# Optimization experiments

Measured on AMD Instinct MI355X. Metric: run time of the kernel, lower is better.

The kernel has to match this reference:

```python
import jax, jax.numpy as jnp
import numpy as np

B, S, H, W, E, NH = 8, 16, 32, 32, 128, 8
HD = E // NH
EPS = 1e-5


def setup_inputs() -> dict:
    key = jax.random.key(0)
    ks = jax.random.split(key, 6)
    sc = lambda fan: 1.0 / np.sqrt(fan).astype(np.float32)
    return {
        "inputs": jax.random.normal(ks[0], (B, S, H, W, E), jnp.float32),
        "W_proj": jax.random.normal(ks[1], (E, E), jnp.float32) * sc(E),
        "ln_gamma": jnp.ones((E,), jnp.float32),
        "ln_beta": jnp.zeros((E,), jnp.float32),
        "W_in": jax.random.normal(ks[2], (E, 3 * E), jnp.float32) * sc(E),
        "W_out": jax.random.normal(ks[3], (E, E), jnp.float32) * sc(E),
        "conv_k": jax.random.normal(ks[4], (4 * E, 2 * E, 3, 3), jnp.float32) * sc(2 * E * 9),
    }


def reference(inputs, W_proj, ln_gamma, ln_beta, W_in, W_out, conv_k):
    # x = silu(project(inputs))
    x = jax.nn.silu(inputs @ W_proj)
    # LayerNorm over last dim
    mu = x.mean(-1, keepdims=True)
    var = x.var(-1, keepdims=True)
    x = (x - mu) * jax.lax.rsqrt(var + EPS) * ln_gamma + ln_beta
    # Multi-head attention over the sequence dim, batched over (b, h, w)
    qkv = (x @ W_in).reshape(B, S, H, W, NH, 3 * HD)
    q, k, v = jnp.split(qkv, 3, axis=-1)
    scale = 1.0 / np.sqrt(HD).astype(np.float32)
    scores = jnp.einsum('bshwid,blhwid->bhwisl', q, k) * scale  # (B,H,W,NH,S,S)
    tril = jnp.tril(jnp.ones((S, S), jnp.float32))
    # faithful to source: +1.0 on/below diagonal, -1000.0 above
    mask = tril * 1.0 + (1.0 - tril) * (-1000.0)
    attnw = jax.nn.softmax(scores + mask, axis=-1)
    ao = jnp.einsum('bhwisl,blhwid->bshwid', attnw, v).reshape(B, S, H, W, E)
    x = ao @ W_out + inputs  # residual
    # ConvLSTM over seq: (B,S,H,W,E) -> (S,B,E,H,W) for scan
    xc = jnp.transpose(x, (1, 0, 4, 2, 3))
    h0 = jnp.zeros((B, E, H, W), x.dtype)
    c0 = jnp.zeros((B, E, H, W), x.dtype)

    def step(carry, xt):
        h, c = carry
        comb = jnp.concatenate([xt, h], axis=1)  # (B, 2E, H, W)
        cc = jax.lax.conv_general_dilated(
            comb, conv_k, window_strides=(1, 1), padding='SAME',
            dimension_numbers=('NCHW', 'OIHW', 'NCHW'))
        ci, cf, co, cg = jnp.split(cc, 4, axis=1)
        c_next = jax.nn.sigmoid(cf) * c + jax.nn.sigmoid(ci) * jnp.tanh(cg)
        h_next = jax.nn.sigmoid(co) * jnp.tanh(c_next)
        return (h_next, c_next), h_next

    _, outs = jax.lax.scan(step, (h0, c0), xc)  # (S,B,E,H,W)
    return jnp.transpose(outs, (1, 0, 3, 4, 2))  # (B,S,H,W,E)
```

## Files before the change

kernel.cpp:

```cpp
#include <hip/hip_runtime.h>
#include <math.h>

#define B_  8
#define S_  16
#define H_  32
#define W_  32
#define E_  128
#define NH_ 8
#define HD_ 16
#define HW_ (H_*W_)
#define NTOK (B_*S_*H_*W_)

typedef __attribute__((ext_vector_type(8))) short short8;
typedef __attribute__((ext_vector_type(4))) short short4v;
typedef __attribute__((ext_vector_type(4))) float floatx4;

__device__ __forceinline__ float sigf(float x){
    return 1.f/(1.f+__expf(-x));
}
__device__ __forceinline__ float tanh_fast(float x){
    x = fminf(fmaxf(x, -15.f), 15.f);
    float e = __expf(2.f*x);
    return (e-1.f)/(e+1.f);
}
__device__ __forceinline__ unsigned short f2bf(float f){
    unsigned int u = __float_as_uint(f);
    u = (u + 0x7fffu + ((u >> 16) & 1u)) >> 16;
    return (unsigned short)u;
}
__device__ __forceinline__ float bf2f(unsigned short h){
    return __uint_as_float(((unsigned int)h) << 16);
}

__device__ __forceinline__ void st_gate(float* p, float v){ *p = v; }
__device__ __forceinline__ void st_gate(unsigned short* p, float v){ *p = f2bf(v); }
__device__ __forceinline__ void load_gate(const float* p, float* o){
    float4 v = *(const float4*)p; o[0]=v.x; o[1]=v.y; o[2]=v.z; o[3]=v.w;
}
__device__ __forceinline__ void load_gate(const unsigned short* p, float* o){
    ushort4 v = *(const ushort4*)p;
    o[0]=bf2f(v.x); o[1]=bf2f(v.y); o[2]=bf2f(v.z); o[3]=bf2f(v.w);
}

__global__ __launch_bounds__(256)
void k_pack_wproj(const float* __restrict__ Wp, short* __restrict__ Wpp){
    int p = blockIdx.x*256 + threadIdx.x;
    int L = p & 63;
    int idx = p >> 6;
    int nt = idx / 12, kb = idx - nt*12;
    int n = nt*16 + (L & 15);
    int kr = (kb & 3)*32 + (L >> 4)*8;
    bool lo = (kb >= 8);
    short8 v;
    #pragma unroll
    for (int j=0;j<8;j++){
        float wv = Wp[(kr+j)*128 + n];
        unsigned short h = f2bf(wv);
        v[j] = lo ? (short)f2bf(wv - bf2f(h)) : (short)h;
    }
    *(short8*)&Wpp[(long)p*8] = v;
}

__global__ __launch_bounds__(256,4)
void k_proj_ln_mfma(const float* __restrict__ in, const short* __restrict__ Wpp,
                    const float* __restrict__ gamma, const float* __restrict__ beta,
                    float* __restrict__ X){
    __shared__ short As[64*264];
    __shared__ float red[4][64][2];
    int tid = threadIdx.x;
    int w = tid >> 6, L = tid & 63;
    int quad = L >> 4, lm = L & 15;
    long r0 = (long)blockIdx.x * 64;

    {
        int c = (tid & 31)*4;
        int rbase = tid >> 5;
        #pragma unroll
        for (int rr=0; rr<8; rr++){
            int r = rr*8 + rbase;
            float4 v = *(const float4*)&in[(r0 + r)*128 + c];
            short4v hv, lv;
            unsigned short h;
            h = f2bf(v.x); hv[0]=(short)h; lv[0]=(short)f2bf(v.x - bf2f(h));
            h = f2bf(v.y); hv[1]=(short)h; lv[1]=(short)f2bf(v.y - bf2f(h));
            h = f2bf(v.z); hv[2]=(short)h; lv[2]=(short)f2bf(v.z - bf2f(h));
            h = f2bf(v.w); hv[3]=(short)h; lv[3]=(short)f2bf(v.w - bf2f(h));
            *(short4v*)&As[r*264 + c] = hv;
            *(short4v*)&As[r*264 + 128 + c] = lv;
        }
    }
    __syncthreads();

    floatx4 acc[4][2];
    #pragma unroll
    for (int mtl=0;mtl<4;mtl++)
        #pragma unroll
        for (int nti=0;nti<2;nti++)
            acc[mtl][nti] = (floatx4){0.f,0.f,0.f,0.f};
    const short8* Bp8 = (const short8*)Wpp;
    #pragma unroll
    for (int kb=0; kb<12; kb++){
        int off = (kb<4) ? kb*32 : ((kb<8) ? 128+(kb-4)*32 : (kb-8)*32);
        short8 af[4];
        #pragma unroll
        for (int mtl=0;mtl<4;mtl++)
            af[mtl] = *(const short8*)&As[(mtl*16+lm)*264 + off + quad*8];
        #pragma unroll
        for (int nti=0;nti<2;nti++){
            short8 bf = Bp8[((2*w+nti)*12+kb)*64 + L];
            #pragma unroll
            for (int mtl=0;mtl<4;mtl++)
                acc[mtl][nti] = __builtin_amdgcn_mfma_f32_16x16x32_bf16(af[mtl], bf, acc[mtl][nti], 0,0,0);
        }
    }

    #pragma unroll
    for (int mtl=0;mtl<4;mtl++){
        float p1[4]={0,0,0,0}, p2[4]={0,0,0,0};
        #pragma unroll
        for (int nti=0;nti<2;nti++)
            #pragma unroll
            for (int r=0;r<4;r++){
                float a = acc[mtl][nti][r];
                float si = a*sigf(a);
                acc[mtl][nti][r] = si;
                p1[r] += si; p2[r] += si*si;
            }
        #pragma unroll
        for (int d=1; d<16; d<<=1)
            #pragma unroll
            for (int r=0;r<4;r++){
                p1[r] += __shfl_xor(p1[r], d);
                p2[r] += __shfl_xor(p2[r], d);
            }
        if (lm == 0){
            #pragma unroll
            for (int r=0;r<4;r++){
                int row = mtl*16 + quad*4 + r;
                red[w][row][0] = p1[r];
                red[w][row][1] = p2[r];
            }
        }
    }
    __syncthreads();
    float g[2], bb[2];
    #pragma unroll
    for (int nti=0;nti<2;nti++){
        g[nti]  = gamma[(2*w+nti)*16 + lm];
        bb[nti] = beta [(2*w+nti)*16 + lm];
    }
    #pragma unroll
    for (int mtl=0;mtl<4;mtl++){
        #pragma unroll
        for (int r=0;r<4;r++){
            int row = mtl*16 + quad*4 + r;
            float s1 = red[0][row][0] + red[1][row][0] + red[2][row][0] + red[3][row][0];
            float s2 = red[0][row][1] + red[1][row][1] + red[2][row][1] + red[3][row][1];
            float mu  = s1 * (1.f/128.f);
            float var = s2 * (1.f/128.f) - mu*mu;
            float rs  = rsqrtf(var + 1e-5f);
            #pragma unroll
            for (int nti=0;nti<2;nti++)
                X[(r0+row)*128 + (2*w+nti)*16 + lm] = (acc[mtl][nti][r]-mu)*rs*g[nti] + bb[nti];
        }
    }
}

__global__ __launch_bounds__(256)
void k_pack_win(const float* __restrict__ Win, short* __restrict__ Winp){
    int p = blockIdx.x*256 + threadIdx.x;
    int L = p & 63;
    int idx = p >> 6;
    int nt = idx >> 2, kc = idx & 3;
    int n = nt*16 + (L & 15);
    int k0 = kc*32 + (L >> 4)*8;
    short8 v;
    #pragma unroll
    for (int j=0;j<8;j++) v[j] = (short)f2bf(Win[(k0+j)*384 + n]);
    *(short8*)&Winp[(long)p*8] = v;
}

__global__ __launch_bounds__(256)
void k_pack_wout(const float* __restrict__ Wout, short* __restrict__ Woutp){
    int p = blockIdx.x*256 + threadIdx.x;
    int L = p & 63;
    int idx = p >> 6;
    int h = idx >> 3, nt = idx & 7;
    int n = nt*16 + (L & 15);
    int k0 = (L >> 4)*8;
    short8 v;
    #pragma unroll
    for (int j=0;j<8;j++){
        int k = k0 + j;
        v[j] = (k < 16) ? (short)f2bf(Wout[(h*16+k)*128 + n]) : (short)0;
    }
    *(short8*)&Woutp[(long)p*8] = v;
}

__global__ __launch_bounds__(256,5)
void k_attn_mfma(const float* __restrict__ X, const short* __restrict__ Winp,
                 const short* __restrict__ Woutp, const float* __restrict__ resid,
                 float* __restrict__ Y){
    __shared__ short lds[16000];
    const int XO=0;
    const int QO=8704;
    const int KO=10240;
    const int VO=11776;
    const int PO=12928;
    const int AOO=14464;
    int tid = threadIdx.x;
    int w = tid >> 6, L = tid & 63;
    int quad = L >> 4, lm = L & 15;
    int b = blockIdx.x >> 8, tile = blockIdx.x & 255;
    int hw0 = tile * 4;
    int hw = hw0 + w;

    {
        int cq = L & 31, rh = L >> 5;
        for (int p=0; p<8; p++){
            int m = w*16 + p*2 + rh;
            int s = m & 15;
            float4 v = *(const float4*)&X[((((long)b*16 + s)*1024) + hw)*128 + cq*4];
            short4v hv;
            hv[0]=(short)f2bf(v.x); hv[1]=(short)f2bf(v.y);
            hv[2]=(short)f2bf(v.z); hv[3]=(short)f2bf(v.w);
            *(short4v*)&lds[XO + m*136 + cq*4] = hv;
        }
    }

    floatx4 Oa[8];
    #pragma unroll
    for (int nt=0;nt<8;nt++) Oa[nt] = (floatx4){0.f,0.f,0.f,0.f};

    const floatx4 zc = (floatx4){0.f,0.f,0.f,0.f};
    const short8 z8 = {0,0,0,0,0,0,0,0};
    int m0 = w*16;

    for (int h=0; h<8; h++){
        floatx4 qacc[3];
        #pragma unroll
        for (int t=0;t<3;t++) qacc[t] = zc;
        #pragma unroll
        for (int kc=0;kc<4;kc++){
            short8 af = *(const short8*)&lds[XO + (m0+lm)*136 + kc*32 + quad*8];
            #pragma unroll
            for (int t=0;t<3;t++){
                int nt = 3*h + t;
                short8 bf = *(const short8*)&Winp[(long)((nt*4+kc)*64 + L)*8];
                qacc[t] = __builtin_amdgcn_mfma_f32_16x16x32_bf16(af, bf, qacc[t], 0,0,0);
            }
        }
        #pragma unroll
        for (int r=0;r<4;r++){
            lds[QO + (m0+quad*4+r)*24 + lm] = (short)f2bf(qacc[0][r]);
            lds[KO + (m0+quad*4+r)*24 + lm] = (short)f2bf(qacc[1][r]);
        }
        {
            short4v vv;
            #pragma unroll
            for (int r=0;r<4;r++) vv[r] = (short)f2bf(qacc[2][r]);
            *(short4v*)&lds[VO + lm*72 + m0 + quad*4] = vv;
        }

        {
            short8 qf = z8, kf = z8;
            if (quad < 2){
                qf = *(const short8*)&lds[QO + (m0+lm)*24 + quad*8];
                kf = *(const short8*)&lds[KO + (m0+lm)*24 + quad*8];
            }
            floatx4 scv = __builtin_amdgcn_mfma_f32_16x16x32_bf16(qf, kf, zc, 0,0,0);
            float pv[4], mr[4];
            #pragma unroll
            for (int r=0;r<4;r++){
                int si = quad*4 + r;
                pv[r] = scv[r]*0.25f + (lm <= si ? 1.0f : -1000.0f);
                mr[r] = pv[r];
            }
            #pragma unroll
            for (int d=1; d<16; d<<=1)
                #pragma unroll
                for (int r=0;r<4;r++) mr[r] = fmaxf(mr[r], __shfl_xor(mr[r], d));
            float ex[4], sm[4];
            #pragma unroll
            for (int r=0;r<4;r++){ ex[r] = __expf(pv[r]-mr[r]); sm[r] = ex[r]; }
            #pragma unroll
            for (int d=1; d<16; d<<=1)
                #pragma unroll
                for (int r=0;r<4;r++) sm[r] += __shfl_xor(sm[r], d);
            #pragma unroll
            for (int r=0;r<4;r++)
                lds[PO + (m0+quad*4+r)*24 + lm] = (short)f2bf(ex[r]/sm[r]);

            short8 pf = z8, vf = z8;
            if (quad < 2){
                pf = *(const short8*)&lds[PO + (m0+lm)*24 + quad*8];
                vf = *(const short8*)&lds[VO + lm*72 + m0 + quad*8];
            }
            floatx4 aov = __builtin_amdgcn_mfma_f32_16x16x32_bf16(pf, vf, zc, 0,0,0);
            #pragma unroll
            for (int r=0;r<4;r++)
                lds[AOO + (m0+quad*4+r)*24 + lm] = (short)f2bf(aov[r]);
        }

        {
            short8 aof = z8;
            if (quad < 2)
                aof = *(const short8*)&lds[AOO + (m0+lm)*24 + quad*8];
            #pragma unroll
            for (int nt=0;nt<8;nt++){
                short8 wf = *(const short8*)&Woutp[(long)((h*8+nt)*64 + L)*8];
                Oa[nt] = __builtin_amdgcn_mfma_f32_16x16x32_bf16(aof, wf, Oa[nt], 0,0,0);
            }
        }
    }

    #pragma unroll
    for (int nt=0;nt<8;nt++){
        int n = nt*16 + lm;
        #pragma unroll
        for (int r=0;r<4;r++){
            int s = quad*4 + r;
            long addr = (((long)b*16 + s)*1024 + hw)*128 + n;
            Y[addr] = Oa[nt][r] + resid[addr];
        }
    }
}

__global__ __launch_bounds__(256)
void k_pack_w(const float* __restrict__ ck, short* __restrict__ Bp){
    int p = blockIdx.x*256 + threadIdx.x;
    int L = p & 63;
    int nt = (p >> 6) & 31;
    int c32 = (p >> 11) & 7;
    int tap = p >> 14;
    int oc = nt*16 + (L & 15);
    int kq = L >> 4;
    short8 v;
    #pragma unroll
    for (int j=0;j<8;j++){
        int ic = c32*32 + kq*8 + j;
        v[j] = (short)f2bf(ck[(oc*256+ic)*9 + tap]);
    }
    *(short8*)&Bp[(long)p*8] = v;
}

__global__ __launch_bounds__(256)
void k_pack_x(const float* __restrict__ X, short* __restrict__ xh, int s, int zero_h){
    int idx = blockIdx.x*256 + threadIdx.x;
    int row = idx >> 4;
    int ch = (idx & 15) * 8;
    int b = row >> 10, hw = row & 1023;
    const float* src = X + (((long)(b*16+s)*1024 + hw)*128 + ch);
    float4 a = *(const float4*)src;
    float4 c = *(const float4*)(src+4);
    short8 v;
    v[0]=(short)f2bf(a.x); v[1]=(short)f2bf(a.y); v[2]=(short)f2bf(a.z); v[3]=(short)f2bf(a.w);
    v[4]=(short)f2bf(c.x); v[5]=(short)f2bf(c.y); v[6]=(short)f2bf(c.z); v[7]=(short)f2bf(c.w);
    *(short8*)&xh[(long)row*256 + ch] = v;
    if (zero_h){
        short8 z = {0,0,0,0,0,0,0,0};
        *(short8*)&xh[(long)row*256 + 128 + ch] = z;
    }
}

template<typename GT>
__global__ __launch_bounds__(512,2)
void k_conv_mfma(const short* __restrict__ xh, const short* __restrict__ Bp,
                 GT* __restrict__ gbuf){
    __shared__ short As[6*34*264];
    int tid = threadIdx.x;
    int Nblk = blockIdx.x & 3, g = blockIdx.x >> 2;
    int b = g >> 3, y0 = (g & 7)*4;
    int w = tid >> 6, L = tid & 63;
    int quad = L >> 4, lm = L & 15;
    int wm = w >> 1, wn = w & 1;
    int ntg = Nblk*8 + wn*4;

    const short8 z8 = {0,0,0,0,0,0,0,0};
    {
        short8 vs[13];
        #pragma unroll
        for (int i=0; i<13; i++){
            int pidx = i*512 + tid;
            short8 v = z8;
            if (pidx < 6528){
                int cb  = pidx & 31;
                int pos = pidx >> 5;
                int row = pos / 34;
                int xp  = pos - row*34;
                int yy = y0 - 1 + row, xx = xp - 1;
                if (yy>=0 && yy<32 && xx>=0 && xx<32)
                    v = *(const short8*)&xh[(((long)(b*32+yy)*32+xx)<<8) + cb*8];
            }
            vs[i] = v;
        }
        #pragma unroll
        for (int i=0; i<13; i++){
            int pidx = i*512 + tid;
            if (pidx < 6528){
                int cb  = pidx & 31;
                int pos = pidx >> 5;
                *(short8*)&As[pos*264 + cb*8] = vs[i];
            }
        }
    }
    __syncthreads();

    floatx4 acc[2][4];
    #pragma unroll
    for (int mtl=0;mtl<2;mtl++)
        #pragma unroll
        for (int nti=0;nti<4;nti++)
            acc[mtl][nti] = (floatx4){0.f,0.f,0.f,0.f};

    const short8* Bp8 = (const short8*)Bp;

    for (int tap=0; tap<9; tap++){
        int dy = tap/3 - 1, dx = tap - (tap/3)*3 - 1;
        int abase[2];
        #pragma unroll
        for (int mtl=0;mtl<2;mtl++){
            int x = mtl*16 + lm;
            abase[mtl] = (((wm+dy+1)*34) + x + dx + 1)*264 + quad*8;
        }
        #pragma unroll
        for (int sic=0; sic<4; sic++){
            #pragma unroll
            for (int c2=0; c2<2; c2++){
                short8 bfr[4];
                #pragma unroll
                for (int nti=0;nti<4;nti++)
                    bfr[nti] = Bp8[((tap*8 + sic*2 + c2)*32 + ntg + nti)*64 + L];
                #pragma unroll
                for (int mtl=0;mtl<2;mtl++){
                    short8 afr = *(const short8*)&As[abase[mtl] + sic*64 + c2*32];
                    #pragma unroll
                    for (int nti=0;nti<4;nti++)
                        acc[mtl][nti] = __builtin_amdgcn_mfma_f32_16x16x32_bf16(afr, bfr[nti], acc[mtl][nti], 0,0,0);
                }
            }
        }
    }

    #pragma unroll
    for (int mtl=0;mtl<2;mtl++){
        #pragma unroll
        for (int nti=0;nti<4;nti++){
            int n = Nblk*128 + (wn*4+nti)*16 + lm;
            #pragma unroll
            for (int r=0;r<4;r++){
                long row = (long)g*128 + wm*32 + mtl*16 + quad*4 + r;
                st_gate(&gbuf[row*512 + n], acc[mtl][nti][r]);
            }
        }
    }
}

template<typename GT>
__global__ __launch_bounds__(256)
void k_lstm(const GT* __restrict__ gbuf, float* __restrict__ cbuf,
            float* __restrict__ X, short* __restrict__ xh, int s){
    int idx = blockIdx.x*256 + threadIdx.x;
    int row = idx >> 5;
    int c4 = (idx & 31)*4;
    float gi[4], gf[4], go[4], gg[4];
    const GT* gp = gbuf + (long)row*512 + c4;
    load_gate(gp,       gi);
    load_gate(gp + 128, gf);
    load_gate(gp + 256, go);
    load_gate(gp + 384, gg);
    float co[4];
    if (s == 0){ co[0]=co[1]=co[2]=co[3]=0.f; }
    else {
        float4 cv = *(const float4*)&cbuf[(long)row*128 + c4];
        co[0]=cv.x; co[1]=cv.y; co[2]=cv.z; co[3]=cv.w;
    }
    float cn[4], hn[4];
    #pragma unroll
    for (int j=0;j<4;j++){
        cn[j] = sigf(gf[j])*co[j] + sigf(gi[j])*tanh_fast(gg[j]);
        hn[j] = sigf(go[j])*tanh_fast(cn[j]);
    }
    *(float4*)&cbuf[(long)row*128 + c4] = make_float4(cn[0],cn[1],cn[2],cn[3]);
    int b = row >> 10, hw = row & 1023;
    long xoff = (((long)(b*16+s)*1024 + hw)*128) + c4;
    *(float4*)&X[xoff] = make_float4(hn[0],hn[1],hn[2],hn[3]);
    ushort4 hv;
    hv.x = f2bf(hn[0]); hv.y = f2bf(hn[1]); hv.z = f2bf(hn[2]); hv.w = f2bf(hn[3]);
    *(ushort4*)&xh[(long)row*256 + 128 + c4] = hv;
    if (s < 15){
        long x2 = (((long)(b*16+s+1)*1024 + hw)*128) + c4;
        float4 xv = *(const float4*)&X[x2];
        ushort4 xb;
        xb.x = f2bf(xv.x); xb.y = f2bf(xv.y); xb.z = f2bf(xv.z); xb.w = f2bf(xv.w);
        *(ushort4*)&xh[(long)row*256 + c4] = xb;
    }
}

extern "C" void kernel_launch(void* const* d_in, const int* in_sizes, int n_in,
                              void* d_out, int out_size, void* d_ws, size_t ws_size,
                              hipStream_t stream){
    const float* inputs = (const float*)d_in[0];
    const float* Wp     = (const float*)d_in[1];
    const float* gamma  = (const float*)d_in[2];
    const float* beta   = (const float*)d_in[3];
    const float* Win    = (const float*)d_in[4];
    const float* Wout   = (const float*)d_in[5];
    const float* ck     = (const float*)d_in[6];
    float* X = (float*)d_out;

    char* ws = (char*)d_ws;
    const size_t szB    = 147456ull*16;
    const size_t szXH   = 8192ull*256*2;
    const size_t szC    = 8192ull*128*4;
    const size_t szWin  = 6144ull*16;
    const size_t szWout = 4096ull*16;
    short* Bp    = (short*)(ws);
    short* xh    = (short*)(ws + szB);
    float* cbuf  = (float*)(ws + szB + szXH);
    short* Winp  = (short*)(ws + szB + szXH + szC);
    short* Woutp = (short*)(ws + szB + szXH + szC + szWin);
    char*  gch   =         ws + szB + szXH + szC + szWin + szWout;
    bool gate_f32 = ws_size >= (szB + szXH + szC + szWin + szWout + 8192ull*512*4);
    short* Wprojp = (short*)gch;

    k_pack_w<<<576, 256, 0, stream>>>(ck, Bp);
    k_pack_win<<<24, 256, 0, stream>>>(Win, Winp);
    k_pack_wout<<<16, 256, 0, stream>>>(Wout, Woutp);
    k_pack_wproj<<<24, 256, 0, stream>>>(Wp, Wprojp);
    k_proj_ln_mfma<<<NTOK/64, 256, 0, stream>>>(inputs, Wprojp, gamma, beta, X);
    k_attn_mfma<<<2048, 256, 0, stream>>>(X, Winp, Woutp, inputs, X);
    k_pack_x<<<512, 256, 0, stream>>>(X, xh, 0, 1);

    if (gate_f32){
        float* gbuf = (float*)gch;
        for (int s=0; s<16; s++){
            k_conv_mfma<float><<<256, 512, 0, stream>>>(xh, Bp, gbuf);
            k_lstm<float><<<1024, 256, 0, stream>>>(gbuf, cbuf, X, xh, s);
        }
    } else {
        unsigned short* gbuf = (unsigned short*)gch;
        for (int s=0; s<16; s++){
            k_conv_mfma<unsigned short><<<256, 512, 0, stream>>>(xh, Bp, gbuf);
            k_lstm<unsigned short><<<1024, 256, 0, stream>>>(gbuf, cbuf, X, xh, s);
        }
    }
}
```

Measured before the change: 859.7 us.

## Fuse ConvLSTM gate convolution with LSTM cell update using ping-pong state buffers

```diff
diff --git a/kernel.cpp b/kernel.cpp
--- a/kernel.cpp
+++ b/kernel.cpp
@@ -30,16 +30,6 @@
 }
 __device__ __forceinline__ float bf2f(unsigned short h){
     return __uint_as_float(((unsigned int)h) << 16);
-}
-
-__device__ __forceinline__ void st_gate(float* p, float v){ *p = v; }
-__device__ __forceinline__ void st_gate(unsigned short* p, float v){ *p = f2bf(v); }
-__device__ __forceinline__ void load_gate(const float* p, float* o){
-    float4 v = *(const float4*)p; o[0]=v.x; o[1]=v.y; o[2]=v.z; o[3]=v.w;
-}
-__device__ __forceinline__ void load_gate(const unsigned short* p, float* o){
-    ushort4 v = *(const ushort4*)p;
-    o[0]=bf2f(v.x); o[1]=bf2f(v.y); o[2]=bf2f(v.z); o[3]=bf2f(v.w);
 }
 
 __global__ __launch_bounds__(256)
@@ -363,10 +353,10 @@
     }
 }
 
-template<typename GT>
 __global__ __launch_bounds__(512,2)
-void k_conv_mfma(const short* __restrict__ xh, const short* __restrict__ Bp,
-                 GT* __restrict__ gbuf){
+void k_conv_lstm(const short* __restrict__ xh_in, const short* __restrict__ Bp,
+                 float* __restrict__ cbuf, float* __restrict__ X,
+                 short* __restrict__ xh_out, int s){
     __shared__ short As[6*34*264];
     int tid = threadIdx.x;
     int Nblk = blockIdx.x & 3, g = blockIdx.x >> 2;
@@ -374,7 +364,6 @@
     int w = tid >> 6, L = tid & 63;
     int quad = L >> 4, lm = L & 15;
     int wm = w >> 1, wn = w & 1;
-    int ntg = Nblk*8 + wn*4;
 
     const short8 z8 = {0,0,0,0,0,0,0,0};
     {
@@ -390,7 +379,7 @@
                 int xp  = pos - row*34;
                 int yy = y0 - 1 + row, xx = xp - 1;
                 if (yy>=0 && yy<32 && xx>=0 && xx<32)
-                    v = *(const short8*)&xh[(((long)(b*32+yy)*32+xx)<<8) + cb*8];
+                    v = *(const short8*)&xh_in[(((long)(b*32+yy)*32+xx)<<8) + cb*8];
             }
             vs[i] = v;
         }
@@ -410,8 +399,8 @@
     #pragma unroll
     for (int mtl=0;mtl<2;mtl++)
         #pragma unroll
-        for (int nti=0;nti<4;nti++)
-            acc[mtl][nti] = (floatx4){0.f,0.f,0.f,0.f};
+        for (int q=0;q<4;q++)
+            acc[mtl][q] = (floatx4){0.f,0.f,0.f,0.f};
 
     const short8* Bp8 = (const short8*)Bp;
 
@@ -429,71 +418,40 @@
             for (int c2=0; c2<2; c2++){
                 short8 bfr[4];
                 #pragma unroll
-                for (int nti=0;nti<4;nti++)
-                    bfr[nti] = Bp8[((tap*8 + sic*2 + c2)*32 + ntg + nti)*64 + L];
+                for (int q=0;q<4;q++)
+                    bfr[q] = Bp8[((tap*8 + sic*2 + c2)*32 + q*8 + Nblk*2 + wn)*64 + L];
                 #pragma unroll
                 for (int mtl=0;mtl<2;mtl++){
                     short8 afr = *(const short8*)&As[abase[mtl] + sic*64 + c2*32];
                     #pragma unroll
-                    for (int nti=0;nti<4;nti++)
-                        acc[mtl][nti] = __builtin_amdgcn_mfma_f32_16x16x32_bf16(afr, bfr[nti], acc[mtl][nti], 0,0,0);
+                    for (int q=0;q<4;q++)
+                        acc[mtl][q] = __builtin_amdgcn_mfma_f32_16x16x32_bf16(afr, bfr[q], acc[mtl][q], 0,0,0);
                 }
             }
         }
     }
 
+    int ch = Nblk*32 + wn*16 + lm;
     #pragma unroll
     for (int mtl=0;mtl<2;mtl++){
         #pragma unroll
-        for (int nti=0;nti<4;nti++){
-            int n = Nblk*128 + (wn*4+nti)*16 + lm;
-            #pragma unroll
-            for (int r=0;r<4;r++){
-                long row = (long)g*128 + wm*32 + mtl*16 + quad*4 + r;
-                st_gate(&gbuf[row*512 + n], acc[mtl][nti][r]);
-            }
-        }
-    }
-}
-
-template<typename GT>
-__global__ __launch_bounds__(256)
-void k_lstm(const GT* __restrict__ gbuf, float* __restrict__ cbuf,
-            float* __restrict__ X, short* __restrict__ xh, int s){
-    int idx = blockIdx.x*256 + threadIdx.x;
-    int row = idx >> 5;
-    int c4 = (idx & 31)*4;
-    float gi[4], gf[4], go[4], gg[4];
-    const GT* gp = gbuf + (long)row*512 + c4;
-    load_gate(gp,       gi);
-    load_gate(gp + 128, gf);
-    load_gate(gp + 256, go);
-    load_gate(gp + 384, gg);
-    float co[4];
-    if (s == 0){ co[0]=co[1]=co[2]=co[3]=0.f; }
-    else {
-        float4 cv = *(const float4*)&cbuf[(long)row*128 + c4];
-        co[0]=cv.x; co[1]=cv.y; co[2]=cv.z; co[3]=cv.w;
-    }
-    float cn[4], hn[4];
-    #pragma unroll
-    for (int j=0;j<4;j++){
-        cn[j] = sigf(gf[j])*co[j] + sigf(gi[j])*tanh_fast(gg[j]);
-        hn[j] = sigf(go[j])*tanh_fast(cn[j]);
-    }
-    *(float4*)&cbuf[(long)row*128 + c4] = make_float4(cn[0],cn[1],cn[2],cn[3]);
-    int b = row >> 10, hw = row & 1023;
-    long xoff = (((long)(b*16+s)*1024 + hw)*128) + c4;
-    *(float4*)&X[xoff] = make_float4(hn[0],hn[1],hn[2],hn[3]);
-    ushort4 hv;
-    hv.x = f2bf(hn[0]); hv.y = f2bf(hn[1]); hv.z = f2bf(hn[2]); hv.w = f2bf(hn[3]);
-    *(ushort4*)&xh[(long)row*256 + 128 + c4] = hv;
-    if (s < 15){
-        long x2 = (((long)(b*16+s+1)*1024 + hw)*128) + c4;
-        float4 xv = *(const float4*)&X[x2];
-        ushort4 xb;
-        xb.x = f2bf(xv.x); xb.y = f2bf(xv.y); xb.z = f2bf(xv.z); xb.w = f2bf(xv.w);
-        *(ushort4*)&xh[(long)row*256 + c4] = xb;
+        for (int r=0;r<4;r++){
+            long row = (long)g*128 + wm*32 + mtl*16 + quad*4 + r;
+            float co = (s == 0) ? 0.f : cbuf[row*128 + ch];
+            float gi = acc[mtl][0][r], gf = acc[mtl][1][r];
+            float go = acc[mtl][2][r], gg = acc[mtl][3][r];
+            float cn = sigf(gf)*co + sigf(gi)*tanh_fast(gg);
+            float hn = sigf(go)*tanh_fast(cn);
+            cbuf[row*128 + ch] = cn;
+            int b2 = (int)(row >> 10), hw = (int)(row & 1023);
+            long xoff = (((long)(b2*16+s)*1024 + hw)*128) + ch;
+            X[xoff] = hn;
+            xh_out[row*256 + 128 + ch] = (short)f2bf(hn);
+            if (s < 15){
+                long x2 = (((long)(b2*16+s+1)*1024 + hw)*128) + ch;
+                xh_out[row*256 + ch] = (short)f2bf(X[x2]);
+            }
+        }
     }
 }
 
@@ -516,13 +474,12 @@
     const size_t szWin  = 6144ull*16;
     const size_t szWout = 4096ull*16;
     short* Bp    = (short*)(ws);
-    short* xh    = (short*)(ws + szB);
+    short* xh0   = (short*)(ws + szB);
     float* cbuf  = (float*)(ws + szB + szXH);
     short* Winp  = (short*)(ws + szB + szXH + szC);
     short* Woutp = (short*)(ws + szB + szXH + szC + szWin);
-    char*  gch   =         ws + szB + szXH + szC + szWin + szWout;
-    bool gate_f32 = ws_size >= (szB + szXH + szC + szWin + szWout + 8192ull*512*4);
-    short* Wprojp = (short*)gch;
+    short* xh1   = (short*)(ws + szB + szXH + szC + szWin + szWout);
+    short* Wprojp= (short*)(ws + szB + szXH + szC + szWin + szWout + szXH);
 
     k_pack_w<<<576, 256, 0, stream>>>(ck, Bp);
     k_pack_win<<<24, 256, 0, stream>>>(Win, Winp);
@@ -530,19 +487,11 @@
     k_pack_wproj<<<24, 256, 0, stream>>>(Wp, Wprojp);
     k_proj_ln_mfma<<<NTOK/64, 256, 0, stream>>>(inputs, Wprojp, gamma, beta, X);
     k_attn_mfma<<<2048, 256, 0, stream>>>(X, Winp, Woutp, inputs, X);
-    k_pack_x<<<512, 256, 0, stream>>>(X, xh, 0, 1);
-
-    if (gate_f32){
-        float* gbuf = (float*)gch;
-        for (int s=0; s<16; s++){
-            k_conv_mfma<float><<<256, 512, 0, stream>>>(xh, Bp, gbuf);
-            k_lstm<float><<<1024, 256, 0, stream>>>(gbuf, cbuf, X, xh, s);
-        }
-    } else {
-        unsigned short* gbuf = (unsigned short*)gch;
-        for (int s=0; s<16; s++){
-            k_conv_mfma<unsigned short><<<256, 512, 0, stream>>>(xh, Bp, gbuf);
-            k_lstm<unsigned short><<<1024, 256, 0, stream>>>(gbuf, cbuf, X, xh, s);
-        }
-    }
-}
+    k_pack_x<<<512, 256, 0, stream>>>(X, xh0, 0, 1);
+
+    for (int s=0; s<16; s++){
+        const short* xin = (s & 1) ? xh1 : xh0;
+        short*       xout= (s & 1) ? xh0 : xh1;
+        k_conv_lstm<<<256, 512, 0, stream>>>(xin, Bp, cbuf, X, xout, s);
+    }
+}
```

After: 940.0 us. 1.09x slower.

## Skip softmax max-reduction, defer normalization, and retile conv warps to 4x2

Applied to the files above, without the earlier changes.

```diff
diff --git a/kernel.cpp b/kernel.cpp
--- a/kernel.cpp
+++ b/kernel.cpp
@@ -269,27 +269,15 @@
                 kf = *(const short8*)&lds[KO + (m0+lm)*24 + quad*8];
             }
             floatx4 scv = __builtin_amdgcn_mfma_f32_16x16x32_bf16(qf, kf, zc, 0,0,0);
-            float pv[4], mr[4];
+            float sm[4];
             #pragma unroll
             for (int r=0;r<4;r++){
                 int si = quad*4 + r;
-                pv[r] = scv[r]*0.25f + (lm <= si ? 1.0f : -1000.0f);
-                mr[r] = pv[r];
-            }
-            #pragma unroll
-            for (int d=1; d<16; d<<=1)
-                #pragma unroll
-                for (int r=0;r<4;r++) mr[r] = fmaxf(mr[r], __shfl_xor(mr[r], d));
-            float ex[4], sm[4];
-            #pragma unroll
-            for (int r=0;r<4;r++){ ex[r] = __expf(pv[r]-mr[r]); sm[r] = ex[r]; }
-            #pragma unroll
-            for (int d=1; d<16; d<<=1)
-                #pragma unroll
-                for (int r=0;r<4;r++) sm[r] += __shfl_xor(sm[r], d);
-            #pragma unroll
-            for (int r=0;r<4;r++)
-                lds[PO + (m0+quad*4+r)*24 + lm] = (short)f2bf(ex[r]/sm[r]);
+                float pv = scv[r]*0.25f + (lm <= si ? 1.0f : -1000.0f);
+                float ex = __expf(pv);
+                sm[r] = ex;
+                lds[PO + (m0+quad*4+r)*24 + lm] = (short)f2bf(ex);
+            }
 
             short8 pf = z8, vf = z8;
             if (quad < 2){
@@ -297,9 +285,16 @@
                 vf = *(const short8*)&lds[VO + lm*72 + m0 + quad*8];
             }
             floatx4 aov = __builtin_amdgcn_mfma_f32_16x16x32_bf16(pf, vf, zc, 0,0,0);
-            #pragma unroll
-            for (int r=0;r<4;r++)
-                lds[AOO + (m0+quad*4+r)*24 + lm] = (short)f2bf(aov[r]);
+
+            #pragma unroll
+            for (int d=1; d<16; d<<=1)
+                #pragma unroll
+                for (int r=0;r<4;r++) sm[r] += __shfl_xor(sm[r], d);
+            #pragma unroll
+            for (int r=0;r<4;r++){
+                float inv = __fdividef(1.0f, sm[r]);
+                lds[AOO + (m0+quad*4+r)*24 + lm] = (short)f2bf(aov[r]*inv);
+            }
         }
 
         {
@@ -373,8 +368,8 @@
     int b = g >> 3, y0 = (g & 7)*4;
     int w = tid >> 6, L = tid & 63;
     int quad = L >> 4, lm = L & 15;
-    int wm = w >> 1, wn = w & 1;
-    int ntg = Nblk*8 + wn*4;
+    int wm = w & 1, wn = w >> 1;
+    int ntg = Nblk*8 + wn*2;
 
     const short8 z8 = {0,0,0,0,0,0,0,0};
     {
@@ -406,36 +401,37 @@
     }
     __syncthreads();
 
-    floatx4 acc[2][4];
-    #pragma unroll
-    for (int mtl=0;mtl<2;mtl++)
-        #pragma unroll
-        for (int nti=0;nti<4;nti++)
+    floatx4 acc[4][2];
+    #pragma unroll
+    for (int mtl=0;mtl<4;mtl++)
+        #pragma unroll
+        for (int nti=0;nti<2;nti++)
             acc[mtl][nti] = (floatx4){0.f,0.f,0.f,0.f};
 
     const short8* Bp8 = (const short8*)Bp;
 
     for (int tap=0; tap<9; tap++){
         int dy = tap/3 - 1, dx = tap - (tap/3)*3 - 1;
-        int abase[2];
-        #pragma unroll
-        for (int mtl=0;mtl<2;mtl++){
-            int x = mtl*16 + lm;
-            abase[mtl] = (((wm+dy+1)*34) + x + dx + 1)*264 + quad*8;
+        int abase[4];
+        #pragma unroll
+        for (int mtl=0;mtl<4;mtl++){
+            int yl = wm*2 + (mtl>>1);
+            int x  = (mtl&1)*16 + lm;
+            abase[mtl] = (((yl+dy+1)*34) + x + dx + 1)*264 + quad*8;
         }
         #pragma unroll
         for (int sic=0; sic<4; sic++){
             #pragma unroll
             for (int c2=0; c2<2; c2++){
-                short8 bfr[4];
+                short8 bfr[2];
                 #pragma unroll
-                for (int nti=0;nti<4;nti++)
+                for (int nti=0;nti<2;nti++)
                     bfr[nti] = Bp8[((tap*8 + sic*2 + c2)*32 + ntg + nti)*64 + L];
                 #pragma unroll
-                for (int mtl=0;mtl<2;mtl++){
+                for (int mtl=0;mtl<4;mtl++){
                     short8 afr = *(const short8*)&As[abase[mtl] + sic*64 + c2*32];
                     #pragma unroll
-                    for (int nti=0;nti<4;nti++)
+                    for (int nti=0;nti<2;nti++)
                         acc[mtl][nti] = __builtin_amdgcn_mfma_f32_16x16x32_bf16(afr, bfr[nti], acc[mtl][nti], 0,0,0);
                 }
             }
@@ -443,13 +439,13 @@
     }
 
     #pragma unroll
-    for (int mtl=0;mtl<2;mtl++){
-        #pragma unroll
-        for (int nti=0;nti<4;nti++){
-            int n = Nblk*128 + (wn*4+nti)*16 + lm;
+    for (int mtl=0;mtl<4;mtl++){
+        #pragma unroll
+        for (int nti=0;nti<2;nti++){
+            int n = Nblk*128 + (wn*2+nti)*16 + lm;
             #pragma unroll
             for (int r=0;r<4;r++){
-                long row = (long)g*128 + wm*32 + mtl*16 + quad*4 + r;
+                long row = (long)g*128 + wm*64 + mtl*16 + quad*4 + r;
                 st_gate(&gbuf[row*512 + n], acc[mtl][nti][r]);
             }
         }
```

After: 870.9 us. Within noise of the previous version (+1.3%).
